# Kernel optimization log

Measured on AMD Instinct MI355X. Metric: run time of the kernel, lower is better.

The kernel has to match this reference:

```python
import jax, jax.numpy as jnp
import numpy as np

L, D = 6, 2048


def setup_inputs() -> dict:
    key = jax.random.key(0)
    ks = jax.random.split(key, 6)
    # 0.05 scale keeps repeated matrix compositions numerically tame
    W_upper = jax.random.normal(ks[0], (L, D, D), dtype=jnp.float32) * 0.05
    W_lower = jax.random.normal(ks[1], (L, D, D), dtype=jnp.float32) * 0.05
    b_upper = jax.random.normal(ks[2], (L, D), dtype=jnp.float32)
    b_lower = jax.random.normal(ks[3], (L, D), dtype=jnp.float32)
    ub = jax.random.normal(ks[4], (L, D), dtype=jnp.float32)
    lb = jax.random.normal(ks[5], (L, D), dtype=jnp.float32)
    return dict(W_upper=W_upper, W_lower=W_lower, b_upper=b_upper,
                b_lower=b_lower, ub=ub, lb=lb)


def _pos(W):
    # M * W  where M = (W >= 0)
    return jnp.where(W >= 0, W, jnp.zeros_like(W))


def _neg(W):
    # ~M * W where M = (W >= 0)
    return jnp.where(W >= 0, jnp.zeros_like(W), W)


def reference(W_upper, W_lower, b_upper, b_lower, ub, lb):
    # Layer index L-1 is `self`; backsubstitute toward layer 0 (input layer).
    Wu, Wl = W_upper[-1], W_lower[-1]          # [D, D]
    bu, bl = b_upper[-1], b_lower[-1]          # [D]
    best_ub, best_lb = ub[-1], lb[-1]          # [D]
    n_layers = W_upper.shape[0]
    for i in range(n_layers - 2, -1, -1):      # prev = layer i
        Wu_p, Wu_n = _pos(Wu), _neg(Wu)
        Wl_p, Wl_n = _pos(Wl), _neg(Wl)
        # concrete bounds through prev's pre-activation bounds
        cur_ub = Wu_p @ ub[i] + Wu_n @ lb[i] + bu
        cur_lb = Wl_p @ lb[i] + Wl_n @ ub[i] + bl
        best_ub = jnp.minimum(best_ub, cur_ub)
        best_lb = jnp.maximum(best_lb, cur_lb)
        # compose symbolic bounds with prev layer's relaxation
        bu = Wu_p @ b_upper[i] + Wu_n @ b_lower[i] + bu
        bl = Wl_p @ b_lower[i] + Wl_n @ b_upper[i] + bl
        Wu = Wu_p @ W_upper[i] + Wu_n @ W_lower[i]
        Wl = Wl_p @ W_lower[i] + Wl_n @ W_upper[i]
    # final concretization against the input layer's bounds (layer 0)
    Wu_p, Wu_n = _pos(Wu), _neg(Wu)
    Wl_p, Wl_n = _pos(Wl), _neg(Wl)
    cur_ub = Wu_p @ ub[0] + Wu_n @ lb[0] + bu
    cur_lb = Wl_p @ lb[0] + Wl_n @ ub[0] + bl
    best_ub = jnp.minimum(best_ub, cur_ub)
    best_lb = jnp.maximum(best_lb, cur_lb)
    return best_ub, best_lb
```

## Files before the change

kernel.cpp:

```cpp
#include <hip/hip_runtime.h>

#define D 2048
#define DD ((size_t)D * (size_t)D)

typedef __attribute__((ext_vector_type(8))) short bf16x8;
typedef __attribute__((ext_vector_type(16))) float f32x16;

#define GLOBAL_AS __attribute__((address_space(1)))
#define LDS_AS __attribute__((address_space(3)))

__device__ inline unsigned short f2bf(float f) {
  unsigned u = __float_as_uint(f);
  u += 0x7fffu + ((u >> 16) & 1u);
  return (unsigned short)(u >> 16);
}
__device__ inline float bf2f(unsigned us) {
  return __uint_as_float(us << 16);
}

__global__ void init_vecs(const float* __restrict__ b_upper5,
                          const float* __restrict__ b_lower5,
                          const float* __restrict__ ub5,
                          const float* __restrict__ lb5,
                          float* __restrict__ bu, float* __restrict__ bl,
                          float* __restrict__ out) {
  int t = blockIdx.x * blockDim.x + threadIdx.x;
  if (t < D) {
    bu[t] = b_upper5[t];
    bl[t] = b_lower5[t];
    out[t] = ub5[t];
    out[D + t] = lb5[t];
  }
}

__global__ __launch_bounds__(256) void prep(
    const float* __restrict__ Wu32, const float* __restrict__ Wl32,
    const unsigned short* __restrict__ WuA, const unsigned short* __restrict__ WlA,
    const float* __restrict__ ubi, const float* __restrict__ lbi,
    const float* __restrict__ bupi, const float* __restrict__ bloi,
    float* __restrict__ bu, float* __restrict__ bl,
    float* __restrict__ best,
    unsigned short* __restrict__ oU, unsigned short* __restrict__ oL,
    const float* __restrict__ Wup, const float* __restrict__ Wlo,
    unsigned short* __restrict__ BsT, unsigned short* __restrict__ BdT,
    int update_bias, int first) {
  __shared__ float red[4][4];
  __shared__ unsigned short sS[64][68];
  __shared__ unsigned short sD[64][68];

  const int t = threadIdx.x;

  if (blockIdx.x < 2048) {
    const int r = blockIdx.x;
    const size_t base = (size_t)r * D + t * 8;
    const int c = t * 8;

    float wu[8], wl[8];
    if (first) {
      float4 wu0 = *(const float4*)(Wu32 + base), wu1 = *(const float4*)(Wu32 + base + 4);
      float4 wl0 = *(const float4*)(Wl32 + base), wl1 = *(const float4*)(Wl32 + base + 4);
      wu[0] = wu0.x; wu[1] = wu0.y; wu[2] = wu0.z; wu[3] = wu0.w;
      wu[4] = wu1.x; wu[5] = wu1.y; wu[6] = wu1.z; wu[7] = wu1.w;
      wl[0] = wl0.x; wl[1] = wl0.y; wl[2] = wl0.z; wl[3] = wl0.w;
      wl[4] = wl1.x; wl[5] = wl1.y; wl[6] = wl1.z; wl[7] = wl1.w;
      uint4 w;
      w.x = f2bf(wu[0]) | ((unsigned)f2bf(wu[1]) << 16);
      w.y = f2bf(wu[2]) | ((unsigned)f2bf(wu[3]) << 16);
      w.z = f2bf(wu[4]) | ((unsigned)f2bf(wu[5]) << 16);
      w.w = f2bf(wu[6]) | ((unsigned)f2bf(wu[7]) << 16);
      *(uint4*)(oU + base) = w;
      w.x = f2bf(wl[0]) | ((unsigned)f2bf(wl[1]) << 16);
      w.y = f2bf(wl[2]) | ((unsigned)f2bf(wl[3]) << 16);
      w.z = f2bf(wl[4]) | ((unsigned)f2bf(wl[5]) << 16);
      w.w = f2bf(wl[6]) | ((unsigned)f2bf(wl[7]) << 16);
      *(uint4*)(oL + base) = w;
    } else {
      uint4 a = *(const uint4*)(WuA + base);
      uint4 b = *(const uint4*)(WlA + base);
      wu[0] = bf2f(a.x & 0xffffu); wu[1] = bf2f(a.x >> 16);
      wu[2] = bf2f(a.y & 0xffffu); wu[3] = bf2f(a.y >> 16);
      wu[4] = bf2f(a.z & 0xffffu); wu[5] = bf2f(a.z >> 16);
      wu[6] = bf2f(a.w & 0xffffu); wu[7] = bf2f(a.w >> 16);
      wl[0] = bf2f(b.x & 0xffffu); wl[1] = bf2f(b.x >> 16);
      wl[2] = bf2f(b.y & 0xffffu); wl[3] = bf2f(b.y >> 16);
      wl[4] = bf2f(b.z & 0xffffu); wl[5] = bf2f(b.z >> 16);
      wl[6] = bf2f(b.w & 0xffffu); wl[7] = bf2f(b.w >> 16);
    }

    float4 u0 = *(const float4*)(ubi + c),  u1 = *(const float4*)(ubi + c + 4);
    float4 l0 = *(const float4*)(lbi + c),  l1 = *(const float4*)(lbi + c + 4);
    float4 p0 = *(const float4*)(bupi + c), p1 = *(const float4*)(bupi + c + 4);
    float4 n0 = *(const float4*)(bloi + c), n1 = *(const float4*)(bloi + c + 4);
    float uu[8] = {u0.x, u0.y, u0.z, u0.w, u1.x, u1.y, u1.z, u1.w};
    float ll[8] = {l0.x, l0.y, l0.z, l0.w, l1.x, l1.y, l1.z, l1.w};
    float pp[8] = {p0.x, p0.y, p0.z, p0.w, p1.x, p1.y, p1.z, p1.w};
    float nn[8] = {n0.x, n0.y, n0.z, n0.w, n1.x, n1.y, n1.z, n1.w};

    float su_c = 0.f, su_b = 0.f, sl_c = 0.f, sl_b = 0.f;
    #pragma unroll
    for (int j = 0; j < 8; ++j) {
      su_c += wu[j] * (wu[j] >= 0.f ? uu[j] : ll[j]);
      su_b += wu[j] * (wu[j] >= 0.f ? pp[j] : nn[j]);
      sl_c += wl[j] * (wl[j] >= 0.f ? ll[j] : uu[j]);
      sl_b += wl[j] * (wl[j] >= 0.f ? nn[j] : pp[j]);
    }

    #pragma unroll
    for (int off = 32; off; off >>= 1) {
      su_c += __shfl_down(su_c, off);
      su_b += __shfl_down(su_b, off);
      sl_c += __shfl_down(sl_c, off);
      sl_b += __shfl_down(sl_b, off);
    }
    int wave = t >> 6;
    if ((t & 63) == 0) {
      red[0][wave] = su_c; red[1][wave] = su_b;
      red[2][wave] = sl_c; red[3][wave] = sl_b;
    }
    __syncthreads();
    if (t == 0) {
      float a = red[0][0] + red[0][1] + red[0][2] + red[0][3];
      float b = red[1][0] + red[1][1] + red[1][2] + red[1][3];
      float cc = red[2][0] + red[2][1] + red[2][2] + red[2][3];
      float d = red[3][0] + red[3][1] + red[3][2] + red[3][3];
      float bu_old = bu[r], bl_old = bl[r];
      best[r]     = fminf(best[r],     a + bu_old);
      best[D + r] = fmaxf(best[D + r], cc + bl_old);
      if (update_bias) {
        bu[r] = b + bu_old;
        bl[r] = d + bl_old;
      }
    }
  } else {
    const int bx = blockIdx.x - 2048;
    const int k0 = (bx >> 5) * 64, c0 = (bx & 31) * 64;
    const int tx = t & 15, ty = t >> 4;
    #pragma unroll
    for (int r = 0; r < 4; ++r) {
      int kk = ty + r * 16;
      size_t g = (size_t)(k0 + kk) * D + c0 + tx * 4;
      float4 up = *(const float4*)(Wup + g);
      float4 lo = *(const float4*)(Wlo + g);
      sS[kk][tx * 4 + 0] = f2bf((up.x + lo.x) * 0.5f);
      sS[kk][tx * 4 + 1] = f2bf((up.y + lo.y) * 0.5f);
      sS[kk][tx * 4 + 2] = f2bf((up.z + lo.z) * 0.5f);
      sS[kk][tx * 4 + 3] = f2bf((up.w + lo.w) * 0.5f);
      sD[kk][tx * 4 + 0] = f2bf((up.x - lo.x) * 0.5f);
      sD[kk][tx * 4 + 1] = f2bf((up.y - lo.y) * 0.5f);
      sD[kk][tx * 4 + 2] = f2bf((up.z - lo.z) * 0.5f);
      sD[kk][tx * 4 + 3] = f2bf((up.w - lo.w) * 0.5f);
    }
    __syncthreads();
    #pragma unroll
    for (int r = 0; r < 4; ++r) {
      int cc = ty + r * 16;
      int kq = tx * 4;
      unsigned a0 = sS[kq + 0][cc] | ((unsigned)sS[kq + 1][cc] << 16);
      unsigned a1 = sS[kq + 2][cc] | ((unsigned)sS[kq + 3][cc] << 16);
      *(uint2*)(BsT + (size_t)(c0 + cc) * D + k0 + kq) = make_uint2(a0, a1);
      a0 = sD[kq + 0][cc] | ((unsigned)sD[kq + 1][cc] << 16);
      a1 = sD[kq + 2][cc] | ((unsigned)sD[kq + 3][cc] << 16);
      *(uint2*)(BdT + (size_t)(c0 + cc) * D + k0 + kq) = make_uint2(a0, a1);
    }
  }
}

__global__ __launch_bounds__(512, 2) void gemm_fused(
    const unsigned short* __restrict__ w16U,
    const unsigned short* __restrict__ w16L,
    const unsigned short* __restrict__ BsT,
    const unsigned short* __restrict__ BdT,
    unsigned short* __restrict__ Cu, unsigned short* __restrict__ Cl) {
  extern __shared__ unsigned char lds[];

  const int bid = blockIdx.x;
  const int vid = (bid & 7) * 32 + (bid >> 3);
  const int row0 = (vid >> 4) * 128, col0 = (vid & 15) * 128;

  const int tid = threadIdx.x;
  const int lane = tid & 63, wid = tid >> 6;
  const int h = wid >> 2;
  const int w2 = wid & 3;
  const int wr = w2 >> 1, wc = w2 & 1;
  const int l31 = lane & 31, kh = lane >> 5;

  const int srow8 = lane >> 3;
  const int slot  = lane & 7;
  int rowc[2], swel[2];
  #pragma unroll
  for (int c = 0; c < 2; ++c) {
    rowc[c] = (wid + c * 8) * 8 + srow8;
    swel[c] = (slot ^ (rowc[c] & 7)) * 8;
  }
  const unsigned short* gAU[2]; const unsigned short* gAL[2];
  const unsigned short* gBs[2]; const unsigned short* gBd[2];
  #pragma unroll
  for (int c = 0; c < 2; ++c) {
    gAU[c] = w16U + (size_t)(row0 + rowc[c]) * D + swel[c];
    gAL[c] = w16L + (size_t)(row0 + rowc[c]) * D + swel[c];
    gBs[c] = BsT + (size_t)(col0 + rowc[c]) * D + swel[c];
    gBd[c] = BdT + (size_t)(col0 + rowc[c]) * D + swel[c];
  }

  f32x16 acc[2][2][2] = {};

  int aoff[2][2], boff[2][2];
  #pragma unroll
  for (int mb = 0; mb < 2; ++mb) {
    int ar = wr * 64 + mb * 32 + l31;
    #pragma unroll
    for (int ksl = 0; ksl < 2; ++ksl)
      aoff[mb][ksl] = ar * 128 + ((((h * 2 + ksl) * 2 + kh) ^ (ar & 7)) * 16);
  }
  #pragma unroll
  for (int nb = 0; nb < 2; ++nb) {
    int bc = wc * 64 + nb * 32 + l31;
    #pragma unroll
    for (int ksl = 0; ksl < 2; ++ksl)
      boff[nb][ksl] = bc * 128 + ((((h * 2 + ksl) * 2 + kh) ^ (bc & 7)) * 16);
  }

  #define STAGE(curb, kt)                                                          \
    do {                                                                           \
      unsigned bb = (unsigned)(curb) * 65536u;                                     \
      _Pragma("unroll")                                                            \
      for (int c = 0; c < 2; ++c) {                                                \
        unsigned dst = bb + (unsigned)(wid + c * 8) * 1024u;                       \
        __builtin_amdgcn_global_load_lds((const GLOBAL_AS unsigned*)(gAU[c] + (kt)),\
            (LDS_AS unsigned*)(lds + 0 + dst), 16, 0, 0);                          \
        __builtin_amdgcn_global_load_lds((const GLOBAL_AS unsigned*)(gAL[c] + (kt)),\
            (LDS_AS unsigned*)(lds + 16384 + dst), 16, 0, 0);                      \
        __builtin_amdgcn_global_load_lds((const GLOBAL_AS unsigned*)(gBs[c] + (kt)),\
            (LDS_AS unsigned*)(lds + 32768 + dst), 16, 0, 0);                      \
        __builtin_amdgcn_global_load_lds((const GLOBAL_AS unsigned*)(gBd[c] + (kt)),\
            (LDS_AS unsigned*)(lds + 49152 + dst), 16, 0, 0);                      \
      }                                                                            \
    } while (0)

  STAGE(0, 0);
  __syncthreads();

  int cur = 0;
  for (int t = 0; t < 32; ++t) {
    if (t < 31) STAGE(cur ^ 1, (t + 1) * 64);

    const unsigned char* Ub = lds + 0 + cur * 65536;
    const unsigned char* Lb = lds + 16384 + cur * 65536;
    const unsigned char* Sb = lds + 32768 + cur * 65536;
    const unsigned char* Db = lds + 49152 + cur * 65536;

    #pragma unroll
    for (int ksl = 0; ksl < 2; ++ksl) {
      bf16x8 au0 = *(const bf16x8*)(Ub + aoff[0][ksl]);
      bf16x8 au1 = *(const bf16x8*)(Ub + aoff[1][ksl]);
      bf16x8 al0 = *(const bf16x8*)(Lb + aoff[0][ksl]);
      bf16x8 al1 = *(const bf16x8*)(Lb + aoff[1][ksl]);
      bf16x8 bs0 = *(const bf16x8*)(Sb + boff[0][ksl]);
      bf16x8 bs1 = *(const bf16x8*)(Sb + boff[1][ksl]);
      bf16x8 bd0 = *(const bf16x8*)(Db + boff[0][ksl]);
      bf16x8 bd1 = *(const bf16x8*)(Db + boff[1][ksl]);

      bf16x8 vu0 = au0 & (short)0x7fff;
      bf16x8 vu1 = au1 & (short)0x7fff;
      bf16x8 vl0 = al0 | (short)0x8000;
      bf16x8 vl1 = al1 | (short)0x8000;

      acc[0][0][0] = __builtin_amdgcn_mfma_f32_32x32x16_bf16(au0, bs0, acc[0][0][0], 0, 0, 0);
      acc[0][0][0] = __builtin_amdgcn_mfma_f32_32x32x16_bf16(vu0, bd0, acc[0][0][0], 0, 0, 0);
      acc[0][0][1] = __builtin_amdgcn_mfma_f32_32x32x16_bf16(au0, bs1, acc[0][0][1], 0, 0, 0);
      acc[0][0][1] = __builtin_amdgcn_mfma_f32_32x32x16_bf16(vu0, bd1, acc[0][0][1], 0, 0, 0);
      acc[0][1][0] = __builtin_amdgcn_mfma_f32_32x32x16_bf16(au1, bs0, acc[0][1][0], 0, 0, 0);
      acc[0][1][0] = __builtin_amdgcn_mfma_f32_32x32x16_bf16(vu1, bd0, acc[0][1][0], 0, 0, 0);
      acc[0][1][1] = __builtin_amdgcn_mfma_f32_32x32x16_bf16(au1, bs1, acc[0][1][1], 0, 0, 0);
      acc[0][1][1] = __builtin_amdgcn_mfma_f32_32x32x16_bf16(vu1, bd1, acc[0][1][1], 0, 0, 0);
      acc[1][0][0] = __builtin_amdgcn_mfma_f32_32x32x16_bf16(al0, bs0, acc[1][0][0], 0, 0, 0);
      acc[1][0][0] = __builtin_amdgcn_mfma_f32_32x32x16_bf16(vl0, bd0, acc[1][0][0], 0, 0, 0);
      acc[1][0][1] = __builtin_amdgcn_mfma_f32_32x32x16_bf16(al0, bs1, acc[1][0][1], 0, 0, 0);
      acc[1][0][1] = __builtin_amdgcn_mfma_f32_32x32x16_bf16(vl0, bd1, acc[1][0][1], 0, 0, 0);
      acc[1][1][0] = __builtin_amdgcn_mfma_f32_32x32x16_bf16(al1, bs0, acc[1][1][0], 0, 0, 0);
      acc[1][1][0] = __builtin_amdgcn_mfma_f32_32x32x16_bf16(vl1, bd0, acc[1][1][0], 0, 0, 0);
      acc[1][1][1] = __builtin_amdgcn_mfma_f32_32x32x16_bf16(al1, bs1, acc[1][1][1], 0, 0, 0);
      acc[1][1][1] = __builtin_amdgcn_mfma_f32_32x32x16_bf16(vl1, bd1, acc[1][1][1], 0, 0, 0);
    }

    __syncthreads();
    cur ^= 1;
  }
  #undef STAGE

  const unsigned rbase = (unsigned)w2 * 32768u + (unsigned)lane * 64u;
  if (h == 1) {
    #pragma unroll
    for (int u = 0; u < 2; ++u)
      #pragma unroll
      for (int mb = 0; mb < 2; ++mb)
        #pragma unroll
        for (int nb = 0; nb < 2; ++nb)
          *(f32x16*)(lds + rbase + (unsigned)(((u * 2 + mb) * 2 + nb)) * 4096u)
              = acc[u][mb][nb];
  }
  __syncthreads();
  if (h == 0) {
    #pragma unroll
    for (int u = 0; u < 2; ++u) {
      unsigned short* C = u ? Cl : Cu;
      #pragma unroll
      for (int mb = 0; mb < 2; ++mb)
        #pragma unroll
        for (int nb = 0; nb < 2; ++nb) {
          f32x16 p = *(const f32x16*)(lds + rbase +
                       (unsigned)(((u * 2 + mb) * 2 + nb)) * 4096u);
          f32x16 s = acc[u][mb][nb] + p;
          const int colg = col0 + wc * 64 + nb * 32 + l31;
          const int rowb = row0 + wr * 64 + mb * 32 + kh * 4;
          #pragma unroll
          for (int g = 0; g < 4; ++g)
            #pragma unroll
            for (int j = 0; j < 4; ++j)
              C[(size_t)(rowb + g * 8 + j) * D + colg] = f2bf(s[g * 4 + j]);
        }
    }
  }
}

extern "C" void kernel_launch(void* const* d_in, const int* in_sizes, int n_in,
                              void* d_out, int out_size, void* d_ws, size_t ws_size,
                              hipStream_t stream) {
  const float* W_upper = (const float*)d_in[0];
  const float* W_lower = (const float*)d_in[1];
  const float* b_upper = (const float*)d_in[2];
  const float* b_lower = (const float*)d_in[3];
  const float* ub      = (const float*)d_in[4];
  const float* lb      = (const float*)d_in[5];
  float* out = (float*)d_out;

  unsigned short* aU[2]; unsigned short* aL[2];
  aU[0] = (unsigned short*)d_ws;
  aL[0] = aU[0] + DD;
  aU[1] = aL[0] + DD;
  aL[1] = aU[1] + DD;
  unsigned short* BsT = aL[1] + DD;
  unsigned short* BdT = BsT + DD;
  float* bu = (float*)(BdT + DD);
  float* bl = bu + D;

  static_cast<void>(hipFuncSetAttribute(
      (const void*)gemm_fused, hipFuncAttributeMaxDynamicSharedMemorySize, 131072));

  init_vecs<<<(D + 255) / 256, 256, 0, stream>>>(
      b_upper + 5 * D, b_lower + 5 * D, ub + 5 * D, lb + 5 * D, bu, bl, out);

  int cur = 0;
  for (int i = 4; i >= 0; --i) {
    const int first = (i == 4);
    prep<<<3072, 256, 0, stream>>>(
        W_upper + 5 * DD, W_lower + 5 * DD,
        aU[cur], aL[cur],
        ub + (size_t)i * D, lb + (size_t)i * D,
        b_upper + (size_t)i * D, b_lower + (size_t)i * D,
        bu, bl, out,
        aU[cur], aL[cur],
        W_upper + (size_t)i * DD, W_lower + (size_t)i * DD,
        BsT, BdT, 1, first);
    gemm_fused<<<256, 512, 131072, stream>>>(aU[cur], aL[cur], BsT, BdT,
                                             aU[cur ^ 1], aL[cur ^ 1]);
    cur ^= 1;
  }
  prep<<<2048, 256, 0, stream>>>(
      (const float*)nullptr, (const float*)nullptr,
      aU[cur], aL[cur],
      ub, lb, b_upper, b_lower, bu, bl, out,
      (unsigned short*)nullptr, (unsigned short*)nullptr,
      (const float*)nullptr, (const float*)nullptr,
      (unsigned short*)nullptr, (unsigned short*)nullptr, 0, 0);
}
```

Measured before the change: 422.3 us.

## Load A operands directly from global into registers, stage only B in LDS

The A tiles (upper/lower weight matrices) are now read straight from global memory into registers with a double-buffered register prefetch, and only the B operands go through LDS via global_load_lds. This halves LDS traffic and footprint per stage and removes the LDS reads for A. The cost is more VGPRs for the prefetched fragments. Each wave also reads A rows from global memory redundantly across waves that share the same rows, which adds L2/global traffic and makes latency hiding depend on register prefetch distance.

```diff
diff --git a/kernel.cpp b/kernel.cpp
--- a/kernel.cpp
+++ b/kernel.cpp
@@ -184,6 +184,10 @@
   const int wr = w2 >> 1, wc = w2 & 1;
   const int l31 = lane & 31, kh = lane >> 5;
 
+  const int aRow = row0 + wr * 64 + l31;
+  const unsigned short* pAU = w16U + (size_t)aRow * D + h * 32 + kh * 8;
+  const unsigned short* pAL = w16L + (size_t)aRow * D + h * 32 + kh * 8;
+
   const int srow8 = lane >> 3;
   const int slot  = lane & 7;
   int rowc[2], swel[2];
@@ -192,26 +196,16 @@
     rowc[c] = (wid + c * 8) * 8 + srow8;
     swel[c] = (slot ^ (rowc[c] & 7)) * 8;
   }
-  const unsigned short* gAU[2]; const unsigned short* gAL[2];
   const unsigned short* gBs[2]; const unsigned short* gBd[2];
   #pragma unroll
   for (int c = 0; c < 2; ++c) {
-    gAU[c] = w16U + (size_t)(row0 + rowc[c]) * D + swel[c];
-    gAL[c] = w16L + (size_t)(row0 + rowc[c]) * D + swel[c];
     gBs[c] = BsT + (size_t)(col0 + rowc[c]) * D + swel[c];
     gBd[c] = BdT + (size_t)(col0 + rowc[c]) * D + swel[c];
   }
 
   f32x16 acc[2][2][2] = {};
 
-  int aoff[2][2], boff[2][2];
-  #pragma unroll
-  for (int mb = 0; mb < 2; ++mb) {
-    int ar = wr * 64 + mb * 32 + l31;
-    #pragma unroll
-    for (int ksl = 0; ksl < 2; ++ksl)
-      aoff[mb][ksl] = ar * 128 + ((((h * 2 + ksl) * 2 + kh) ^ (ar & 7)) * 16);
-  }
+  int boff[2][2];
   #pragma unroll
   for (int nb = 0; nb < 2; ++nb) {
     int bc = wc * 64 + nb * 32 + l31;
@@ -220,73 +214,84 @@
       boff[nb][ksl] = bc * 128 + ((((h * 2 + ksl) * 2 + kh) ^ (bc & 7)) * 16);
   }
 
-  #define STAGE(curb, kt)                                                          \
+  #define STAGE_B(bufb, kt)                                                        \
     do {                                                                           \
-      unsigned bb = (unsigned)(curb) * 65536u;                                     \
       _Pragma("unroll")                                                            \
       for (int c = 0; c < 2; ++c) {                                                \
-        unsigned dst = bb + (unsigned)(wid + c * 8) * 1024u;                       \
-        __builtin_amdgcn_global_load_lds((const GLOBAL_AS unsigned*)(gAU[c] + (kt)),\
+        unsigned dst = (unsigned)(bufb) * 32768u + (unsigned)(wid + c * 8) * 1024u;\
+        __builtin_amdgcn_global_load_lds((const GLOBAL_AS unsigned*)(gBs[c] + (kt)),\
             (LDS_AS unsigned*)(lds + 0 + dst), 16, 0, 0);                          \
-        __builtin_amdgcn_global_load_lds((const GLOBAL_AS unsigned*)(gAL[c] + (kt)),\
+        __builtin_amdgcn_global_load_lds((const GLOBAL_AS unsigned*)(gBd[c] + (kt)),\
             (LDS_AS unsigned*)(lds + 16384 + dst), 16, 0, 0);                      \
-        __builtin_amdgcn_global_load_lds((const GLOBAL_AS unsigned*)(gBs[c] + (kt)),\
-            (LDS_AS unsigned*)(lds + 32768 + dst), 16, 0, 0);                      \
-        __builtin_amdgcn_global_load_lds((const GLOBAL_AS unsigned*)(gBd[c] + (kt)),\
-            (LDS_AS unsigned*)(lds + 49152 + dst), 16, 0, 0);                      \
       }                                                                            \
     } while (0)
 
-  STAGE(0, 0);
+  #define LOADA(au, al, kt)                                                        \
+    do {                                                                           \
+      _Pragma("unroll")                                                            \
+      for (int mb = 0; mb < 2; ++mb)                                               \
+        _Pragma("unroll")                                                          \
+        for (int ksl = 0; ksl < 2; ++ksl) {                                        \
+          au[mb][ksl] = *(const bf16x8*)(pAU + (size_t)mb * 32 * D + ksl * 16 + (kt)); \
+          al[mb][ksl] = *(const bf16x8*)(pAL + (size_t)mb * 32 * D + ksl * 16 + (kt)); \
+        }                                                                          \
+    } while (0)
+
+  #define COMPUTE(au, al, bufb)                                                    \
+    do {                                                                           \
+      const unsigned char* Sb = lds + (unsigned)(bufb) * 32768u;                   \
+      const unsigned char* Db = Sb + 16384;                                        \
+      _Pragma("unroll")                                                            \
+      for (int ksl = 0; ksl < 2; ++ksl) {                                          \
+        bf16x8 bs0 = *(const bf16x8*)(Sb + boff[0][ksl]);                          \
+        bf16x8 bs1 = *(const bf16x8*)(Sb + boff[1][ksl]);                          \
+        bf16x8 bd0 = *(const bf16x8*)(Db + boff[0][ksl]);                          \
+        bf16x8 bd1 = *(const bf16x8*)(Db + boff[1][ksl]);                          \
+        bf16x8 vu0 = au[0][ksl] & (short)0x7fff;                                   \
+        bf16x8 vu1 = au[1][ksl] & (short)0x7fff;                                   \
+        bf16x8 vl0 = al[0][ksl] | (short)0x8000;                                   \
+        bf16x8 vl1 = al[1][ksl] | (short)0x8000;                                   \
+        acc[0][0][0] = __builtin_amdgcn_mfma_f32_32x32x16_bf16(au[0][ksl], bs0, acc[0][0][0], 0, 0, 0); \
+        acc[0][0][0] = __builtin_amdgcn_mfma_f32_32x32x16_bf16(vu0,        bd0, acc[0][0][0], 0, 0, 0); \
+        acc[0][0][1] = __builtin_amdgcn_mfma_f32_32x32x16_bf16(au[0][ksl], bs1, acc[0][0][1], 0, 0, 0); \
+        acc[0][0][1] = __builtin_amdgcn_mfma_f32_32x32x16_bf16(vu0,        bd1, acc[0][0][1], 0, 0, 0); \
+        acc[0][1][0] = __builtin_amdgcn_mfma_f32_32x32x16_bf16(au[1][ksl], bs0, acc[0][1][0], 0, 0, 0); \
+        acc[0][1][0] = __builtin_amdgcn_mfma_f32_32x32x16_bf16(vu1,        bd0, acc[0][1][0], 0, 0, 0); \
+        acc[0][1][1] = __builtin_amdgcn_mfma_f32_32x32x16_bf16(au[1][ksl], bs1, acc[0][1][1], 0, 0, 0); \
+        acc[0][1][1] = __builtin_amdgcn_mfma_f32_32x32x16_bf16(vu1,        bd1, acc[0][1][1], 0, 0, 0); \
+        acc[1][0][0] = __builtin_amdgcn_mfma_f32_32x32x16_bf16(al[0][ksl], bs0, acc[1][0][0], 0, 0, 0); \
+        acc[1][0][0] = __builtin_amdgcn_mfma_f32_32x32x16_bf16(vl0,        bd0, acc[1][0][0], 0, 0, 0); \
+        acc[1][0][1] = __builtin_amdgcn_mfma_f32_32x32x16_bf16(al[0][ksl], bs1, acc[1][0][1], 0, 0, 0); \
+        acc[1][0][1] = __builtin_amdgcn_mfma_f32_32x32x16_bf16(vl0,        bd1, acc[1][0][1], 0, 0, 0); \
+        acc[1][1][0] = __builtin_amdgcn_mfma_f32_32x32x16_bf16(al[1][ksl], bs0, acc[1][1][0], 0, 0, 0); \
+        acc[1][1][0] = __builtin_amdgcn_mfma_f32_32x32x16_bf16(vl1,        bd0, acc[1][1][0], 0, 0, 0); \
+        acc[1][1][1] = __builtin_amdgcn_mfma_f32_32x32x16_bf16(al[1][ksl], bs1, acc[1][1][1], 0, 0, 0); \
+        acc[1][1][1] = __builtin_amdgcn_mfma_f32_32x32x16_bf16(vl1,        bd1, acc[1][1][1], 0, 0, 0); \
+      }                                                                            \
+    } while (0)
+
+  bf16x8 auA[2][2], alA[2][2], auB[2][2], alB[2][2];
+
+  LOADA(auA, alA, 0);
+  STAGE_B(0, 0);
   __syncthreads();
 
-  int cur = 0;
-  for (int t = 0; t < 32; ++t) {
-    if (t < 31) STAGE(cur ^ 1, (t + 1) * 64);
-
-    const unsigned char* Ub = lds + 0 + cur * 65536;
-    const unsigned char* Lb = lds + 16384 + cur * 65536;
-    const unsigned char* Sb = lds + 32768 + cur * 65536;
-    const unsigned char* Db = lds + 49152 + cur * 65536;
-
-    #pragma unroll
-    for (int ksl = 0; ksl < 2; ++ksl) {
-      bf16x8 au0 = *(const bf16x8*)(Ub + aoff[0][ksl]);
-      bf16x8 au1 = *(const bf16x8*)(Ub + aoff[1][ksl]);
-      bf16x8 al0 = *(const bf16x8*)(Lb + aoff[0][ksl]);
-      bf16x8 al1 = *(const bf16x8*)(Lb + aoff[1][ksl]);
-      bf16x8 bs0 = *(const bf16x8*)(Sb + boff[0][ksl]);
-      bf16x8 bs1 = *(const bf16x8*)(Sb + boff[1][ksl]);
-      bf16x8 bd0 = *(const bf16x8*)(Db + boff[0][ksl]);
-      bf16x8 bd1 = *(const bf16x8*)(Db + boff[1][ksl]);
-
-      bf16x8 vu0 = au0 & (short)0x7fff;
-      bf16x8 vu1 = au1 & (short)0x7fff;
-      bf16x8 vl0 = al0 | (short)0x8000;
-      bf16x8 vl1 = al1 | (short)0x8000;
-
-      acc[0][0][0] = __builtin_amdgcn_mfma_f32_32x32x16_bf16(au0, bs0, acc[0][0][0], 0, 0, 0);
-      acc[0][0][0] = __builtin_amdgcn_mfma_f32_32x32x16_bf16(vu0, bd0, acc[0][0][0], 0, 0, 0);
-      acc[0][0][1] = __builtin_amdgcn_mfma_f32_32x32x16_bf16(au0, bs1, acc[0][0][1], 0, 0, 0);
-      acc[0][0][1] = __builtin_amdgcn_mfma_f32_32x32x16_bf16(vu0, bd1, acc[0][0][1], 0, 0, 0);
-      acc[0][1][0] = __builtin_amdgcn_mfma_f32_32x32x16_bf16(au1, bs0, acc[0][1][0], 0, 0, 0);
-      acc[0][1][0] = __builtin_amdgcn_mfma_f32_32x32x16_bf16(vu1, bd0, acc[0][1][0], 0, 0, 0);
-      acc[0][1][1] = __builtin_amdgcn_mfma_f32_32x32x16_bf16(au1, bs1, acc[0][1][1], 0, 0, 0);
-      acc[0][1][1] = __builtin_amdgcn_mfma_f32_32x32x16_bf16(vu1, bd1, acc[0][1][1], 0, 0, 0);
-      acc[1][0][0] = __builtin_amdgcn_mfma_f32_32x32x16_bf16(al0, bs0, acc[1][0][0], 0, 0, 0);
-      acc[1][0][0] = __builtin_amdgcn_mfma_f32_32x32x16_bf16(vl0, bd0, acc[1][0][0], 0, 0, 0);
-      acc[1][0][1] = __builtin_amdgcn_mfma_f32_32x32x16_bf16(al0, bs1, acc[1][0][1], 0, 0, 0);
-      acc[1][0][1] = __builtin_amdgcn_mfma_f32_32x32x16_bf16(vl0, bd1, acc[1][0][1], 0, 0, 0);
-      acc[1][1][0] = __builtin_amdgcn_mfma_f32_32x32x16_bf16(al1, bs0, acc[1][1][0], 0, 0, 0);
-      acc[1][1][0] = __builtin_amdgcn_mfma_f32_32x32x16_bf16(vl1, bd0, acc[1][1][0], 0, 0, 0);
-      acc[1][1][1] = __builtin_amdgcn_mfma_f32_32x32x16_bf16(al1, bs1, acc[1][1][1], 0, 0, 0);
-      acc[1][1][1] = __builtin_amdgcn_mfma_f32_32x32x16_bf16(vl1, bd1, acc[1][1][1], 0, 0, 0);
-    }
-
+  #pragma unroll 1
+  for (int t = 0; t < 32; t += 2) {
+    LOADA(auB, alB, (t + 1) * 64);
+    STAGE_B(1, (t + 1) * 64);
+    COMPUTE(auA, alA, 0);
     __syncthreads();
-    cur ^= 1;
-  }
-  #undef STAGE
+    if (t + 2 < 32) {
+      LOADA(auA, alA, (t + 2) * 64);
+      STAGE_B(0, (t + 2) * 64);
+    }
+    COMPUTE(auB, alB, 1);
+    __syncthreads();
+  }
+  #undef STAGE_B
+  #undef LOADA
+  #undef COMPUTE
 
   const unsigned rbase = (unsigned)w2 * 32768u + (unsigned)lane * 64u;
   if (h == 1) {
```

Measured after the change: 555.5 us. +31.5%, slower.

## Fuse bound concretization matvecs into GEMM epilogue with atomic row reductions

Applied to the files above, without the earlier changes.

The per-row concretization and bias-composition matvecs (positive/negative split times ub/lb and biases) move from a separate prep pass, which reread the full bf16 composed matrices each layer, into the GEMM epilogue. The epilogue uses the fp32 accumulators it already holds, reduces across lanes with shuffles and accumulates partial row sums into a workspace with atomicAdd. A small finalize pass then applies min/max and the bias updates and clears the accumulators. This removes a full D×D read per layer, at the cost of atomic contention, extra epilogue registers, and sign tests now taken on fp32 values instead of bf16-rounded ones.

```diff
diff --git a/kernel.cpp b/kernel.cpp
--- a/kernel.cpp
+++ b/kernel.cpp
@@ -23,27 +23,26 @@
                           const float* __restrict__ ub5,
                           const float* __restrict__ lb5,
                           float* __restrict__ bu, float* __restrict__ bl,
-                          float* __restrict__ out) {
+                          float* __restrict__ out, float* __restrict__ acc4) {
   int t = blockIdx.x * blockDim.x + threadIdx.x;
   if (t < D) {
     bu[t] = b_upper5[t];
     bl[t] = b_lower5[t];
     out[t] = ub5[t];
     out[D + t] = lb5[t];
-  }
-}
-
-__global__ __launch_bounds__(256) void prep(
+    acc4[t] = 0.f; acc4[D + t] = 0.f; acc4[2 * D + t] = 0.f; acc4[3 * D + t] = 0.f;
+  }
+}
+
+__global__ __launch_bounds__(256) void prep_full(
     const float* __restrict__ Wu32, const float* __restrict__ Wl32,
-    const unsigned short* __restrict__ WuA, const unsigned short* __restrict__ WlA,
     const float* __restrict__ ubi, const float* __restrict__ lbi,
     const float* __restrict__ bupi, const float* __restrict__ bloi,
     float* __restrict__ bu, float* __restrict__ bl,
     float* __restrict__ best,
     unsigned short* __restrict__ oU, unsigned short* __restrict__ oL,
     const float* __restrict__ Wup, const float* __restrict__ Wlo,
-    unsigned short* __restrict__ BsT, unsigned short* __restrict__ BdT,
-    int update_bias, int first) {
+    unsigned short* __restrict__ BsT, unsigned short* __restrict__ BdT) {
   __shared__ float red[4][4];
   __shared__ unsigned short sS[64][68];
   __shared__ unsigned short sD[64][68];
@@ -55,37 +54,22 @@
     const size_t base = (size_t)r * D + t * 8;
     const int c = t * 8;
 
-    float wu[8], wl[8];
-    if (first) {
-      float4 wu0 = *(const float4*)(Wu32 + base), wu1 = *(const float4*)(Wu32 + base + 4);
-      float4 wl0 = *(const float4*)(Wl32 + base), wl1 = *(const float4*)(Wl32 + base + 4);
-      wu[0] = wu0.x; wu[1] = wu0.y; wu[2] = wu0.z; wu[3] = wu0.w;
-      wu[4] = wu1.x; wu[5] = wu1.y; wu[6] = wu1.z; wu[7] = wu1.w;
-      wl[0] = wl0.x; wl[1] = wl0.y; wl[2] = wl0.z; wl[3] = wl0.w;
-      wl[4] = wl1.x; wl[5] = wl1.y; wl[6] = wl1.z; wl[7] = wl1.w;
-      uint4 w;
-      w.x = f2bf(wu[0]) | ((unsigned)f2bf(wu[1]) << 16);
-      w.y = f2bf(wu[2]) | ((unsigned)f2bf(wu[3]) << 16);
-      w.z = f2bf(wu[4]) | ((unsigned)f2bf(wu[5]) << 16);
-      w.w = f2bf(wu[6]) | ((unsigned)f2bf(wu[7]) << 16);
-      *(uint4*)(oU + base) = w;
-      w.x = f2bf(wl[0]) | ((unsigned)f2bf(wl[1]) << 16);
-      w.y = f2bf(wl[2]) | ((unsigned)f2bf(wl[3]) << 16);
-      w.z = f2bf(wl[4]) | ((unsigned)f2bf(wl[5]) << 16);
-      w.w = f2bf(wl[6]) | ((unsigned)f2bf(wl[7]) << 16);
-      *(uint4*)(oL + base) = w;
-    } else {
-      uint4 a = *(const uint4*)(WuA + base);
-      uint4 b = *(const uint4*)(WlA + base);
-      wu[0] = bf2f(a.x & 0xffffu); wu[1] = bf2f(a.x >> 16);
-      wu[2] = bf2f(a.y & 0xffffu); wu[3] = bf2f(a.y >> 16);
-      wu[4] = bf2f(a.z & 0xffffu); wu[5] = bf2f(a.z >> 16);
-      wu[6] = bf2f(a.w & 0xffffu); wu[7] = bf2f(a.w >> 16);
-      wl[0] = bf2f(b.x & 0xffffu); wl[1] = bf2f(b.x >> 16);
-      wl[2] = bf2f(b.y & 0xffffu); wl[3] = bf2f(b.y >> 16);
-      wl[4] = bf2f(b.z & 0xffffu); wl[5] = bf2f(b.z >> 16);
-      wl[6] = bf2f(b.w & 0xffffu); wl[7] = bf2f(b.w >> 16);
-    }
+    float4 wu0 = *(const float4*)(Wu32 + base), wu1 = *(const float4*)(Wu32 + base + 4);
+    float4 wl0 = *(const float4*)(Wl32 + base), wl1 = *(const float4*)(Wl32 + base + 4);
+    float wu[8] = {wu0.x, wu0.y, wu0.z, wu0.w, wu1.x, wu1.y, wu1.z, wu1.w};
+    float wl[8] = {wl0.x, wl0.y, wl0.z, wl0.w, wl1.x, wl1.y, wl1.z, wl1.w};
+
+    uint4 w;
+    w.x = f2bf(wu[0]) | ((unsigned)f2bf(wu[1]) << 16);
+    w.y = f2bf(wu[2]) | ((unsigned)f2bf(wu[3]) << 16);
+    w.z = f2bf(wu[4]) | ((unsigned)f2bf(wu[5]) << 16);
+    w.w = f2bf(wu[6]) | ((unsigned)f2bf(wu[7]) << 16);
+    *(uint4*)(oU + base) = w;
+    w.x = f2bf(wl[0]) | ((unsigned)f2bf(wl[1]) << 16);
+    w.y = f2bf(wl[2]) | ((unsigned)f2bf(wl[3]) << 16);
+    w.z = f2bf(wl[4]) | ((unsigned)f2bf(wl[5]) << 16);
+    w.w = f2bf(wl[6]) | ((unsigned)f2bf(wl[7]) << 16);
+    *(uint4*)(oL + base) = w;
 
     float4 u0 = *(const float4*)(ubi + c),  u1 = *(const float4*)(ubi + c + 4);
     float4 l0 = *(const float4*)(lbi + c),  l1 = *(const float4*)(lbi + c + 4);
@@ -126,10 +110,8 @@
       float bu_old = bu[r], bl_old = bl[r];
       best[r]     = fminf(best[r],     a + bu_old);
       best[D + r] = fmaxf(best[D + r], cc + bl_old);
-      if (update_bias) {
-        bu[r] = b + bu_old;
-        bl[r] = d + bl_old;
-      }
+      bu[r] = b + bu_old;
+      bl[r] = d + bl_old;
     }
   } else {
     const int bx = blockIdx.x - 2048;
@@ -165,12 +147,69 @@
   }
 }
 
+__global__ __launch_bounds__(256) void prep_conv(
+    const float* __restrict__ Wup, const float* __restrict__ Wlo,
+    unsigned short* __restrict__ BsT, unsigned short* __restrict__ BdT,
+    float* __restrict__ acc4, float* __restrict__ bu, float* __restrict__ bl,
+    float* __restrict__ best, int nconv, int update_bias) {
+  const int t = threadIdx.x;
+  if ((int)blockIdx.x >= nconv) {
+    const int r = ((int)blockIdx.x - nconv) * 256 + t;
+    float su_c = acc4[r], su_b = acc4[D + r];
+    float sl_c = acc4[2 * D + r], sl_b = acc4[3 * D + r];
+    float bu_old = bu[r], bl_old = bl[r];
+    best[r]     = fminf(best[r],     su_c + bu_old);
+    best[D + r] = fmaxf(best[D + r], sl_c + bl_old);
+    if (update_bias) {
+      bu[r] = su_b + bu_old;
+      bl[r] = sl_b + bl_old;
+    }
+    acc4[r] = 0.f; acc4[D + r] = 0.f; acc4[2 * D + r] = 0.f; acc4[3 * D + r] = 0.f;
+    return;
+  }
+  __shared__ unsigned short sS[64][68];
+  __shared__ unsigned short sD[64][68];
+  const int bx = blockIdx.x;
+  const int k0 = (bx >> 5) * 64, c0 = (bx & 31) * 64;
+  const int tx = t & 15, ty = t >> 4;
+  #pragma unroll
+  for (int r = 0; r < 4; ++r) {
+    int kk = ty + r * 16;
+    size_t g = (size_t)(k0 + kk) * D + c0 + tx * 4;
+    float4 up = *(const float4*)(Wup + g);
+    float4 lo = *(const float4*)(Wlo + g);
+    sS[kk][tx * 4 + 0] = f2bf((up.x + lo.x) * 0.5f);
+    sS[kk][tx * 4 + 1] = f2bf((up.y + lo.y) * 0.5f);
+    sS[kk][tx * 4 + 2] = f2bf((up.z + lo.z) * 0.5f);
+    sS[kk][tx * 4 + 3] = f2bf((up.w + lo.w) * 0.5f);
+    sD[kk][tx * 4 + 0] = f2bf((up.x - lo.x) * 0.5f);
+    sD[kk][tx * 4 + 1] = f2bf((up.y - lo.y) * 0.5f);
+    sD[kk][tx * 4 + 2] = f2bf((up.z - lo.z) * 0.5f);
+    sD[kk][tx * 4 + 3] = f2bf((up.w - lo.w) * 0.5f);
+  }
+  __syncthreads();
+  #pragma unroll
+  for (int r = 0; r < 4; ++r) {
+    int cc = ty + r * 16;
+    int kq = tx * 4;
+    unsigned a0 = sS[kq + 0][cc] | ((unsigned)sS[kq + 1][cc] << 16);
+    unsigned a1 = sS[kq + 2][cc] | ((unsigned)sS[kq + 3][cc] << 16);
+    *(uint2*)(BsT + (size_t)(c0 + cc) * D + k0 + kq) = make_uint2(a0, a1);
+    a0 = sD[kq + 0][cc] | ((unsigned)sD[kq + 1][cc] << 16);
+    a1 = sD[kq + 2][cc] | ((unsigned)sD[kq + 3][cc] << 16);
+    *(uint2*)(BdT + (size_t)(c0 + cc) * D + k0 + kq) = make_uint2(a0, a1);
+  }
+}
+
 __global__ __launch_bounds__(512, 2) void gemm_fused(
     const unsigned short* __restrict__ w16U,
     const unsigned short* __restrict__ w16L,
     const unsigned short* __restrict__ BsT,
     const unsigned short* __restrict__ BdT,
-    unsigned short* __restrict__ Cu, unsigned short* __restrict__ Cl) {
+    unsigned short* __restrict__ Cu, unsigned short* __restrict__ Cl,
+    const float* __restrict__ ubn, const float* __restrict__ lbn,
+    const float* __restrict__ bpn, const float* __restrict__ bnn,
+    float* __restrict__ acc4, int do_bias) {
   extern __shared__ unsigned char lds[];
 
   const int bid = blockIdx.x;
@@ -302,22 +341,73 @@
   __syncthreads();
   if (h == 0) {
     #pragma unroll
+    for (int u = 0; u < 2; ++u)
+      #pragma unroll
+      for (int mb = 0; mb < 2; ++mb)
+        #pragma unroll
+        for (int nb = 0; nb < 2; ++nb)
+          acc[u][mb][nb] += *(const f32x16*)(lds + rbase +
+                              (unsigned)(((u * 2 + mb) * 2 + nb)) * 4096u);
+
+    #pragma unroll
     for (int u = 0; u < 2; ++u) {
       unsigned short* C = u ? Cl : Cu;
       #pragma unroll
       for (int mb = 0; mb < 2; ++mb)
         #pragma unroll
         for (int nb = 0; nb < 2; ++nb) {
-          f32x16 p = *(const f32x16*)(lds + rbase +
-                       (unsigned)(((u * 2 + mb) * 2 + nb)) * 4096u);
-          f32x16 s = acc[u][mb][nb] + p;
           const int colg = col0 + wc * 64 + nb * 32 + l31;
           const int rowb = row0 + wr * 64 + mb * 32 + kh * 4;
           #pragma unroll
           for (int g = 0; g < 4; ++g)
             #pragma unroll
             for (int j = 0; j < 4; ++j)
-              C[(size_t)(rowb + g * 8 + j) * D + colg] = f2bf(s[g * 4 + j]);
+              C[(size_t)(rowb + g * 8 + j) * D + colg] = f2bf(acc[u][mb][nb][g * 4 + j]);
+        }
+    }
+
+    float ubv[2], lbv[2], bpv[2], bnv[2];
+    #pragma unroll
+    for (int nb = 0; nb < 2; ++nb) {
+      const int colg = col0 + wc * 64 + nb * 32 + l31;
+      ubv[nb] = ubn[colg];
+      lbv[nb] = lbn[colg];
+      bpv[nb] = do_bias ? bpn[colg] : 0.f;
+      bnv[nb] = do_bias ? bnn[colg] : 0.f;
+    }
+    #pragma unroll
+    for (int mb = 0; mb < 2; ++mb) {
+      const int rowb = row0 + wr * 64 + mb * 32 + kh * 4;
+      #pragma unroll
+      for (int g = 0; g < 4; ++g)
+        #pragma unroll
+        for (int j = 0; j < 4; ++j) {
+          float cu_c = 0.f, cu_b = 0.f, cl_c = 0.f, cl_b = 0.f;
+          #pragma unroll
+          for (int nb = 0; nb < 2; ++nb) {
+            float su = acc[0][mb][nb][g * 4 + j];
+            float sl = acc[1][mb][nb][g * 4 + j];
+            cu_c += su * (su >= 0.f ? ubv[nb] : lbv[nb]);
+            cl_c += sl * (sl >= 0.f ? lbv[nb] : ubv[nb]);
+            cu_b += su * (su >= 0.f ? bpv[nb] : bnv[nb]);
+            cl_b += sl * (sl >= 0.f ? bnv[nb] : bpv[nb]);
+          }
+          #pragma unroll
+          for (int off = 16; off; off >>= 1) {
+            cu_c += __shfl_down(cu_c, off, 32);
+            cl_c += __shfl_down(cl_c, off, 32);
+            cu_b += __shfl_down(cu_b, off, 32);
+            cl_b += __shfl_down(cl_b, off, 32);
+          }
+          if (l31 == 0) {
+            const int row = rowb + g * 8 + j;
+            atomicAdd(&acc4[row], cu_c);
+            atomicAdd(&acc4[2 * D + row], cl_c);
+            if (do_bias) {
+              atomicAdd(&acc4[D + row], cu_b);
+              atomicAdd(&acc4[3 * D + row], cl_b);
+            }
+          }
         }
     }
   }
@@ -343,34 +433,37 @@
   unsigned short* BdT = BsT + DD;
   float* bu = (float*)(BdT + DD);
   float* bl = bu + D;
+  float* acc4 = bl + D;
 
   static_cast<void>(hipFuncSetAttribute(
       (const void*)gemm_fused, hipFuncAttributeMaxDynamicSharedMemorySize, 131072));
 
   init_vecs<<<(D + 255) / 256, 256, 0, stream>>>(
-      b_upper + 5 * D, b_lower + 5 * D, ub + 5 * D, lb + 5 * D, bu, bl, out);
+      b_upper + 5 * D, b_lower + 5 * D, ub + 5 * D, lb + 5 * D, bu, bl, out, acc4);
+
+  prep_full<<<3072, 256, 0, stream>>>(
+      W_upper + 5 * DD, W_lower + 5 * DD,
+      ub + 4 * (size_t)D, lb + 4 * (size_t)D,
+      b_upper + 4 * (size_t)D, b_lower + 4 * (size_t)D,
+      bu, bl, out, aU[0], aL[0],
+      W_upper + 4 * DD, W_lower + 4 * DD, BsT, BdT);
 
   int cur = 0;
   for (int i = 4; i >= 0; --i) {
-    const int first = (i == 4);
-    prep<<<3072, 256, 0, stream>>>(
-        W_upper + 5 * DD, W_lower + 5 * DD,
-        aU[cur], aL[cur],
-        ub + (size_t)i * D, lb + (size_t)i * D,
-        b_upper + (size_t)i * D, b_lower + (size_t)i * D,
-        bu, bl, out,
-        aU[cur], aL[cur],
-        W_upper + (size_t)i * DD, W_lower + (size_t)i * DD,
-        BsT, BdT, 1, first);
-    gemm_fused<<<256, 512, 131072, stream>>>(aU[cur], aL[cur], BsT, BdT,
-                                             aU[cur ^ 1], aL[cur ^ 1]);
+    if (i < 4) {
+      prep_conv<<<1032, 256, 0, stream>>>(
+          W_upper + (size_t)i * DD, W_lower + (size_t)i * DD, BsT, BdT,
+          acc4, bu, bl, out, 1024, 1);
+    }
+    const size_t vix = (i >= 1 ? (size_t)(i - 1) : 0) * D;
+    gemm_fused<<<256, 512, 131072, stream>>>(
+        aU[cur], aL[cur], BsT, BdT, aU[cur ^ 1], aL[cur ^ 1],
+        ub + vix, lb + vix, b_upper + vix, b_lower + vix,
+        acc4, (i >= 1) ? 1 : 0);
     cur ^= 1;
   }
-  prep<<<2048, 256, 0, stream>>>(
+  prep_conv<<<8, 256, 0, stream>>>(
       (const float*)nullptr, (const float*)nullptr,
-      aU[cur], aL[cur],
-      ub, lb, b_upper, b_lower, bu, bl, out,
       (unsigned short*)nullptr, (unsigned short*)nullptr,
-      (const float*)nullptr, (const float*)nullptr,
-      (unsigned short*)nullptr, (unsigned short*)nullptr, 0, 0);
-}
+      acc4, bu, bl, out, 0, 0);
+}
```

Result: slower. 455.2 us (+7.8%).
